# Kernel tuning notes

Hardware: AMD Instinct MI355X
Metric: run time of the kernel (lower is better)

## Reference

```python
import jax, jax.numpy as jnp
import numpy as np

DIM = 1024
CTX_DIM = 768
HEADS = 16
D_HEAD = 64
INNER = HEADS * D_HEAD  # 1024
EPS = 1e-5


def _layernorm(x, g, b):
    mu = jnp.mean(x, axis=-1, keepdims=True)
    var = jnp.mean(jnp.square(x - mu), axis=-1, keepdims=True)
    return (x - mu) * jax.lax.rsqrt(var + EPS) * g + b


def setup_inputs() -> dict:
    key = jax.random.key(0)
    ks = jax.random.split(key, 8)
    s = lambda fan_in: 1.0 / np.sqrt(fan_in)
    return {
        "x": jax.random.normal(ks[0], (4, 2048, DIM), dtype=jnp.float32),
        "context": jax.random.normal(ks[1], (4, 2048, CTX_DIM), dtype=jnp.float32),
        "norm_g": jnp.ones((DIM,), jnp.float32),
        "norm_b": jnp.zeros((DIM,), jnp.float32),
        "normc_g": jnp.ones((CTX_DIM,), jnp.float32),
        "normc_b": jnp.zeros((CTX_DIM,), jnp.float32),
        # Linear weights stored [in, out] so y = x @ W (bias=False as in module)
        "Wq": jax.random.uniform(ks[2], (DIM, INNER), jnp.float32, -s(DIM), s(DIM)),
        "Wk": jax.random.uniform(ks[3], (CTX_DIM, INNER), jnp.float32, -s(CTX_DIM), s(CTX_DIM)),
        "Wv": jax.random.uniform(ks[4], (CTX_DIM, INNER), jnp.float32, -s(CTX_DIM), s(CTX_DIM)),
        "Wo": jax.random.uniform(ks[5], (INNER, DIM), jnp.float32, -s(INNER), s(INNER)),
    }


def reference(x, context, norm_g, norm_b, normc_g, normc_b, Wq, Wk, Wv, Wo):
    b, n, _ = x.shape
    m = context.shape[1]
    xn = _layernorm(x, norm_g, norm_b)
    cn = _layernorm(context, normc_g, normc_b)
    # project and split heads: b n (h d) -> b h n d
    split = lambda t, L: t.reshape(b, L, HEADS, D_HEAD).transpose(0, 2, 1, 3)
    q = split(xn @ Wq, n)
    k = split(cn @ Wk, m)
    v = split(cn @ Wv, m)
    sim = jnp.einsum('bhid,bhjd->bhij', q, k) / np.sqrt(D_HEAD)
    attn = jax.nn.softmax(sim, axis=-1)  # dropout p=0 (eval): identity
    out = jnp.einsum('bhij,bhjd->bhid', attn, v)
    out = out.transpose(0, 2, 1, 3).reshape(b, n, INNER)
    return out @ Wo
```

## Files before the change

### kernel.cpp

```cpp
#include <hip/hip_runtime.h>
#include <hip/hip_bf16.h>
#include <stdint.h>

#define TOK 8192
#define NQ 2048
#define DIMX 1024
#define CTXD 768

typedef __attribute__((ext_vector_type(8))) short short8;
typedef __attribute__((ext_vector_type(4))) float f32x4;
typedef __attribute__((ext_vector_type(2))) unsigned int u32x2;

typedef __attribute__((address_space(3))) uint32_t lds_u32_t;
typedef const __attribute__((address_space(1))) uint32_t glb_u32_t;

__device__ __forceinline__ void gld_lds16(const void* g, void* l) {
  __builtin_amdgcn_global_load_lds((glb_u32_t*)g, (lds_u32_t*)l, 16, 0, 0);
}

__device__ __forceinline__ uint16_t f2bf(float f) {
  union { float f; uint32_t u; } v; v.f = f;
  uint32_t r = v.u + 0x7fffu + ((v.u >> 16) & 1u);
  return (uint16_t)(r >> 16);
}

__device__ __forceinline__ uint32_t cvt_pk_bf16(float lo, float hi) {
  uint32_t d;
  asm("v_cvt_pk_bf16_f32 %0, %1, %2" : "=v"(d) : "v"(lo), "v"(hi));
  return d;
}

__device__ __forceinline__ float fexp2(float x) {
#if __has_builtin(__builtin_amdgcn_exp2f)
  return __builtin_amdgcn_exp2f(x);
#else
  float d;
  asm volatile("v_exp_f32 %0, %1\n\ts_nop 1" : "=v"(d) : "v"(x));
  return d;
#endif
}

template<int COLS, int NW>
__global__ __launch_bounds__(COLS/4)
void ln_cast_kernel(const float* __restrict__ x, const float* __restrict__ g,
                    const float* __restrict__ b, uint16_t* __restrict__ out) {
  int row = blockIdx.x;
  int tid = threadIdx.x;
  const float* xr = x + (size_t)row * COLS + tid * 4;
  float4 v = *(const float4*)xr;
  float s1 = v.x + v.y + v.z + v.w;
  float s2 = v.x*v.x + v.y*v.y + v.z*v.z + v.w*v.w;
#pragma unroll
  for (int off = 1; off < 64; off <<= 1) {
    s1 += __shfl_xor(s1, off);
    s2 += __shfl_xor(s2, off);
  }
  __shared__ float sm[2][NW];
  int w = tid >> 6;
  if ((tid & 63) == 0) { sm[0][w] = s1; sm[1][w] = s2; }
  __syncthreads();
  float t1 = 0.f, t2 = 0.f;
#pragma unroll
  for (int i = 0; i < NW; i++) { t1 += sm[0][i]; t2 += sm[1][i]; }
  float mu = t1 * (1.0f / COLS);
  float var = t2 * (1.0f / COLS) - mu * mu;
  float rs = rsqrtf(var + 1e-5f);
  float4 gv = *(const float4*)(g + tid * 4);
  float4 bv = *(const float4*)(b + tid * 4);
  uint32_t lo = (uint32_t)f2bf((v.x - mu) * rs * gv.x + bv.x) |
                ((uint32_t)f2bf((v.y - mu) * rs * gv.y + bv.y) << 16);
  uint32_t hi = (uint32_t)f2bf((v.z - mu) * rs * gv.z + bv.z) |
                ((uint32_t)f2bf((v.w - mu) * rs * gv.w + bv.w) << 16);
  uint2 o; o.x = lo; o.y = hi;
  *(uint2*)(out + (size_t)row * COLS + tid * 4) = o;
}

__global__ __launch_bounds__(256)
void transpose_cast4_kernel(const float* __restrict__ W0, const float* __restrict__ W1,
                            const float* __restrict__ W2, const float* __restrict__ W3,
                            uint16_t* __restrict__ T0, uint16_t* __restrict__ T1,
                            uint16_t* __restrict__ T2, uint16_t* __restrict__ T3) {
  int z = blockIdx.z;
  const float* W = (z == 0) ? W0 : (z == 1) ? W1 : (z == 2) ? W2 : W3;
  uint16_t* WT   = (z == 0) ? T0 : (z == 1) ? T1 : (z == 2) ? T2 : T3;
  int K = (z == 1 || z == 2) ? CTXD : DIMX;
  const int N = DIMX;
  int c0 = blockIdx.x * 32, r0 = blockIdx.y * 32;
  if (r0 >= K) return;
  __shared__ float t[32][33];
  int tx = threadIdx.x & 31, ty = threadIdx.x >> 5;
#pragma unroll
  for (int i = 0; i < 4; i++)
    t[ty + 8*i][tx] = W[(size_t)(r0 + ty + 8*i) * N + c0 + tx];
  __syncthreads();
#pragma unroll
  for (int i = 0; i < 4; i++)
    WT[(size_t)(c0 + ty + 8*i) * K + r0 + tx] = f2bf(t[tx][ty + 8*i]);
}

__device__ __forceinline__ void gemm_block(
    const uint16_t* __restrict__ A, const uint16_t* __restrict__ BT,
    void* __restrict__ C, int N, int K, float oscale,
    int out_bf16, int permc, int m0, int n0,
    uint16_t* Al, uint16_t* Bl, int tid) {
  int l = tid & 63, w = tid >> 6;
  int g = l >> 4, r = l & 15;
  int wm = w >> 1, wn = w & 1;
  f32x4 acc[4][4] = {};
  int srow = tid >> 3, sslot = tid & 7;

  for (int kt = 0; kt < K; kt += 64) {
    __syncthreads();
#pragma unroll
    for (int c = 0; c < 4; c++) {
      int row = c * 32 + srow;
      int ksrc = (sslot * 8) ^ ((row & 7) << 3);
      gld_lds16(A + (size_t)(m0 + row) * K + kt + ksrc, Al + (c * 256 + w * 64) * 8);
    }
#pragma unroll
    for (int c = 0; c < 4; c++) {
      int row = c * 32 + srow;
      int ksrc = (sslot * 8) ^ ((row & 7) << 3);
      gld_lds16(BT + (size_t)(n0 + row) * K + kt + ksrc, Bl + (c * 256 + w * 64) * 8);
    }
    __syncthreads();
#pragma unroll
    for (int kk = 0; kk < 2; kk++) {
      int kb2 = (kk * 32 + g * 8) * 2;
      short8 af[4], bfr[4];
#pragma unroll
      for (int mf = 0; mf < 4; mf++) {
        int row = wm * 64 + mf * 16 + r;
        af[mf] = *(const short8*)((const char*)Al + row * 128 + (kb2 ^ ((row & 7) << 4)));
      }
#pragma unroll
      for (int nf = 0; nf < 4; nf++) {
        int row = wn * 64 + nf * 16 + r;
        bfr[nf] = *(const short8*)((const char*)Bl + row * 128 + (kb2 ^ ((row & 7) << 4)));
      }
#pragma unroll
      for (int mf = 0; mf < 4; mf++)
#pragma unroll
        for (int nf = 0; nf < 4; nf++)
          acc[mf][nf] = __builtin_amdgcn_mfma_f32_16x16x32_bf16(af[mf], bfr[nf], acc[mf][nf], 0, 0, 0);
    }
  }
#pragma unroll
  for (int mf = 0; mf < 4; mf++) {
#pragma unroll
    for (int i = 0; i < 4; i++) {
      size_t row = (size_t)m0 + wm * 64 + mf * 16 + g * 4 + i;
      if (permc) {
        u32x2 pk;
        pk.x = cvt_pk_bf16(acc[mf][0][i], acc[mf][1][i]);
        pk.y = cvt_pk_bf16(acc[mf][2][i], acc[mf][3][i]);
        *(u32x2*)((uint16_t*)C + row * N + n0 + wn * 64 + r * 4) = pk;
      } else {
#pragma unroll
        for (int nf = 0; nf < 4; nf++) {
          int col = n0 + wn * 64 + nf * 16 + r;
          float val = acc[mf][nf][i] * oscale;
          if (out_bf16) ((uint16_t*)C)[row * N + col] = f2bf(val);
          else          ((float*)C)[row * N + col] = val;
        }
      }
    }
  }
}

__global__ __launch_bounds__(256)
void gemm_proj3_kernel(const uint16_t* __restrict__ xn, const uint16_t* __restrict__ cn,
                       const uint16_t* __restrict__ WqT, const uint16_t* __restrict__ WkT,
                       const uint16_t* __restrict__ WvT,
                       uint16_t* __restrict__ Qs, uint16_t* __restrict__ Ks,
                       uint16_t* __restrict__ VTs, float qscale) {
  __shared__ __align__(16) uint16_t Al[128 * 64];
  __shared__ __align__(16) uint16_t Bl[128 * 64];
  int flat = blockIdx.x;
  flat = (flat & 7) * 192 + (flat >> 3);
  const uint16_t* A; const uint16_t* BT; uint16_t* C;
  int N, K, permc, m0, n0;
  float osc = 1.f;
  if (flat < 512) {
    A = xn; BT = WqT; C = Qs; N = DIMX; K = DIMX; permc = 0; osc = qscale;
    n0 = (flat & 7) * 128; m0 = (flat >> 3) * 128;
  } else if (flat < 1024) {
    int f = flat - 512;
    A = cn; BT = WkT; C = Ks; N = DIMX; K = CTXD; permc = 0;
    n0 = (f & 7) * 128; m0 = (f >> 3) * 128;
  } else {
    int f = flat - 1024;
    A = WvT; BT = cn; C = VTs; N = TOK; K = CTXD; permc = 1;
    n0 = (f & 63) * 128; m0 = (f >> 6) * 128;
  }
  gemm_block(A, BT, C, N, K, osc, 1, permc, m0, n0, Al, Bl, threadIdx.x);
}

__global__ __launch_bounds__(256)
void gemm_out_kernel(const uint16_t* __restrict__ A, const uint16_t* __restrict__ BT,
                     float* __restrict__ C, int M, int N, int K) {
  __shared__ __align__(16) uint16_t Al[128 * 64];
  __shared__ __align__(16) uint16_t Bl[128 * 64];
  int flat = blockIdx.y * gridDim.x + blockIdx.x;
  int nwg = gridDim.x * gridDim.y;
  flat = (flat & 7) * (nwg >> 3) + (flat >> 3);
  int bx = flat & (gridDim.x - 1);
  int by = flat / gridDim.x;
  gemm_block(A, BT, C, N, K, 1.f, 0, 0, by * 128, bx * 128, Al, Bl, threadIdx.x);
}

__global__ __launch_bounds__(256)
void attn_kernel(const uint16_t* __restrict__ Q, const uint16_t* __restrict__ Kp,
                 const uint16_t* __restrict__ VT, uint16_t* __restrict__ O) {
  __shared__ __align__(16) uint16_t Kl[64 * 64];
  __shared__ __align__(16) uint16_t Vl[64 * 64];
  __shared__ __align__(16) uint16_t Pl[4 * 32 * 64];
  int tid = threadIdx.x;
  int l = tid & 63, w = tid >> 6;
  int g = l >> 4, r = l & 15;
  int flat = blockIdx.y * 16 + blockIdx.x;
  flat = (flat & 7) * 128 + (flat >> 3);
  int q0 = (flat & 15) * 128;
  int bh = flat >> 4, b = bh >> 4, h = bh & 15;

  short8 qa[2][2];
#pragma unroll
  for (int qb = 0; qb < 2; qb++) {
    const uint16_t* qptr = Q + (size_t)(b * NQ + q0 + w * 32 + qb * 16 + r) * DIMX + h * 64;
    qa[qb][0] = *(const short8*)(qptr + g * 8);
    qa[qb][1] = *(const short8*)(qptr + 32 + g * 8);
  }

  float lpart[2][4] = {};
  f32x4 oacc[2][4] = {};

  const uint16_t* kbase = Kp + (size_t)(b * NQ) * DIMX + h * 64;
  const uint16_t* vbase = VT + (size_t)(h * 64) * TOK + b * NQ;
  int srow = tid >> 3, sslot = tid & 7;

  char* pwb = (char*)Pl + w * 4096;
  const char* prb = (const char*)Pl + w * 4096;

  for (int kv0 = 0; kv0 < NQ; kv0 += 64) {
    __syncthreads();
#pragma unroll
    for (int c = 0; c < 2; c++) {
      int key = c * 32 + srow;
      int dsrc = (sslot * 8) ^ ((key & 7) << 3);
      gld_lds16(kbase + (size_t)(kv0 + key) * DIMX + dsrc, Kl + (c * 256 + w * 64) * 8);
    }
#pragma unroll
    for (int c = 0; c < 2; c++) {
      int d = c * 32 + srow;
      int ksrc = (sslot * 8) ^ ((d & 7) << 3);
      gld_lds16(vbase + (size_t)d * TOK + kv0 + ksrc, Vl + (c * 256 + w * 64) * 8);
    }
    __syncthreads();

    f32x4 sc[2][4] = {};
    __builtin_amdgcn_s_setprio(1);
#pragma unroll
    for (int kk = 0; kk < 2; kk++) {
      int kb2 = (kk * 32 + g * 8) * 2;
#pragma unroll
      for (int c = 0; c < 4; c++) {
        int row = c * 16 + r;
        short8 kf = *(const short8*)((const char*)Kl + row * 128 + (kb2 ^ ((row & 7) << 4)));
        sc[0][c] = __builtin_amdgcn_mfma_f32_16x16x32_bf16(qa[0][kk], kf, sc[0][c], 0, 0, 0);
        sc[1][c] = __builtin_amdgcn_mfma_f32_16x16x32_bf16(qa[1][kk], kf, sc[1][c], 0, 0, 0);
      }
    }
    __builtin_amdgcn_s_setprio(0);

#pragma unroll
    for (int qb = 0; qb < 2; qb++) {
#pragma unroll
      for (int i = 0; i < 4; i++) {
        float p0 = fexp2(sc[qb][0][i]);
        float p1 = fexp2(sc[qb][1][i]);
        float p2 = fexp2(sc[qb][2][i]);
        float p3 = fexp2(sc[qb][3][i]);
        lpart[qb][i] += (p0 + p1) + (p2 + p3);
        u32x2 pk;
        pk.x = cvt_pk_bf16(p0, p1);
        pk.y = cvt_pk_bf16(p2, p3);
        int q = qb * 16 + g * 4 + i;
        *(u32x2*)(pwb + q * 128 + ((r * 8) ^ ((q & 7) << 4))) = pk;
      }
    }

    __builtin_amdgcn_s_setprio(1);
#pragma unroll
    for (int kk = 0; kk < 2; kk++) {
      int kb2 = (kk * 64 + g * 16);
      short8 pa0 = *(const short8*)(prb + (0 * 16 + r) * 128 + (kb2 ^ ((r & 7) << 4)));
      short8 pa1 = *(const short8*)(prb + (1 * 16 + r) * 128 + (kb2 ^ ((r & 7) << 4)));
#pragma unroll
      for (int c = 0; c < 4; c++) {
        int row = c * 16 + r;
        short8 vf = *(const short8*)((const char*)Vl + row * 128 + ((kk * 32 + g * 8) * 2 ^ ((row & 7) << 4)));
        oacc[0][c] = __builtin_amdgcn_mfma_f32_16x16x32_bf16(pa0, vf, oacc[0][c], 0, 0, 0);
        oacc[1][c] = __builtin_amdgcn_mfma_f32_16x16x32_bf16(pa1, vf, oacc[1][c], 0, 0, 0);
      }
    }
    __builtin_amdgcn_s_setprio(0);
  }

#pragma unroll
  for (int qb = 0; qb < 2; qb++)
#pragma unroll
    for (int i = 0; i < 4; i++) {
      lpart[qb][i] += __shfl_xor(lpart[qb][i], 1);
      lpart[qb][i] += __shfl_xor(lpart[qb][i], 2);
      lpart[qb][i] += __shfl_xor(lpart[qb][i], 4);
      lpart[qb][i] += __shfl_xor(lpart[qb][i], 8);
    }

#pragma unroll
  for (int qb = 0; qb < 2; qb++) {
    uint16_t* obase = O + (size_t)(b * NQ + q0 + w * 32 + qb * 16) * DIMX + h * 64;
#pragma unroll
    for (int i = 0; i < 4; i++) {
      float inv = 1.f / lpart[qb][i];
#pragma unroll
      for (int c = 0; c < 4; c++)
        obase[(size_t)(g * 4 + i) * DIMX + c * 16 + r] = f2bf(oacc[qb][c][i] * inv);
    }
  }
}

extern "C" void kernel_launch(void* const* d_in, const int* in_sizes, int n_in,
                              void* d_out, int out_size, void* d_ws, size_t ws_size,
                              hipStream_t stream) {
  (void)in_sizes; (void)n_in; (void)out_size; (void)ws_size;
  const float* x       = (const float*)d_in[0];
  const float* ctx     = (const float*)d_in[1];
  const float* norm_g  = (const float*)d_in[2];
  const float* norm_b  = (const float*)d_in[3];
  const float* normc_g = (const float*)d_in[4];
  const float* normc_b = (const float*)d_in[5];
  const float* Wq      = (const float*)d_in[6];
  const float* Wk      = (const float*)d_in[7];
  const float* Wv      = (const float*)d_in[8];
  const float* Wo      = (const float*)d_in[9];

  char* p = (char*)d_ws;
  uint16_t* xn  = (uint16_t*)p; p += (size_t)TOK * DIMX * 2;
  uint16_t* cn  = (uint16_t*)p; p += (size_t)TOK * CTXD * 2;
  uint16_t* WqT = (uint16_t*)p; p += (size_t)DIMX * DIMX * 2;
  uint16_t* WkT = (uint16_t*)p; p += (size_t)DIMX * CTXD * 2;
  uint16_t* WvT = (uint16_t*)p; p += (size_t)DIMX * CTXD * 2;
  uint16_t* WoT = (uint16_t*)p; p += (size_t)DIMX * DIMX * 2;
  uint16_t* Qs  = (uint16_t*)p; p += (size_t)TOK * DIMX * 2;
  uint16_t* Ks  = (uint16_t*)p; p += (size_t)TOK * DIMX * 2;
  uint16_t* VTs = (uint16_t*)p; p += (size_t)DIMX * TOK * 2;
  uint16_t* AO  = (uint16_t*)p; p += (size_t)TOK * DIMX * 2;

  ln_cast_kernel<DIMX, 4><<<TOK, 256, 0, stream>>>(x, norm_g, norm_b, xn);
  ln_cast_kernel<CTXD, 3><<<TOK, 192, 0, stream>>>(ctx, normc_g, normc_b, cn);

  transpose_cast4_kernel<<<dim3(DIMX/32, DIMX/32, 4), 256, 0, stream>>>(
      Wq, Wk, Wv, Wo, WqT, WkT, WvT, WoT);

  const float qscale = 0.125f * 1.44269504088896340736f;
  gemm_proj3_kernel<<<1536, 256, 0, stream>>>(xn, cn, WqT, WkT, WvT, Qs, Ks, VTs, qscale);

  attn_kernel<<<dim3(NQ/128, 64), 256, 0, stream>>>(Qs, Ks, VTs, AO);

  gemm_out_kernel<<<dim3(DIMX/128, TOK/128), 256, 0, stream>>>(AO, WoT, (float*)d_out, TOK, DIMX, DIMX);
}
```

Before: 206.4 us.

## Merge layernorm launches and use 128x64 tiles in output projection GEMM

The two layernorm launches become a single kernel over both x and context rows. For context rows, threads past the 768 columns sit idle. The output projection GEMM gets its own inline 128x64 tile loop instead of the shared 128x128 gemm_block, which doubles the workgroup count from 512 to 1024 so more CUs stay busy. The cost is more A-tile reloads from memory, and each workgroup does less compute per byte loaded.

```diff
diff --git a/kernel.cpp b/kernel.cpp
--- a/kernel.cpp
+++ b/kernel.cpp
@@ -40,14 +40,20 @@
 #endif
 }
 
-template<int COLS, int NW>
-__global__ __launch_bounds__(COLS/4)
-void ln_cast_kernel(const float* __restrict__ x, const float* __restrict__ g,
-                    const float* __restrict__ b, uint16_t* __restrict__ out) {
+__global__ __launch_bounds__(256)
+void ln_both_kernel(const float* __restrict__ x, const float* __restrict__ gx,
+                    const float* __restrict__ bx,
+                    const float* __restrict__ c, const float* __restrict__ gc,
+                    const float* __restrict__ bc,
+                    uint16_t* __restrict__ xn, uint16_t* __restrict__ cn) {
   int row = blockIdx.x;
   int tid = threadIdx.x;
-  const float* xr = x + (size_t)row * COLS + tid * 4;
-  float4 v = *(const float4*)xr;
+  const float *src, *g, *bb; uint16_t* dst; int COLS;
+  if (row < TOK) { src = x; g = gx; bb = bx; dst = xn; COLS = DIMX; }
+  else { row -= TOK; src = c; g = gc; bb = bc; dst = cn; COLS = CTXD; }
+  bool act = tid * 4 < COLS;
+  float4 v = make_float4(0.f, 0.f, 0.f, 0.f);
+  if (act) v = *(const float4*)(src + (size_t)row * COLS + tid * 4);
   float s1 = v.x + v.y + v.z + v.w;
   float s2 = v.x*v.x + v.y*v.y + v.z*v.z + v.w*v.w;
 #pragma unroll
@@ -55,24 +61,25 @@
     s1 += __shfl_xor(s1, off);
     s2 += __shfl_xor(s2, off);
   }
-  __shared__ float sm[2][NW];
+  __shared__ float sm[2][4];
   int w = tid >> 6;
   if ((tid & 63) == 0) { sm[0][w] = s1; sm[1][w] = s2; }
   __syncthreads();
-  float t1 = 0.f, t2 = 0.f;
-#pragma unroll
-  for (int i = 0; i < NW; i++) { t1 += sm[0][i]; t2 += sm[1][i]; }
-  float mu = t1 * (1.0f / COLS);
-  float var = t2 * (1.0f / COLS) - mu * mu;
+  float t1 = sm[0][0] + sm[0][1] + sm[0][2] + sm[0][3];
+  float t2 = sm[1][0] + sm[1][1] + sm[1][2] + sm[1][3];
+  float mu = t1 / COLS;
+  float var = t2 / COLS - mu * mu;
   float rs = rsqrtf(var + 1e-5f);
-  float4 gv = *(const float4*)(g + tid * 4);
-  float4 bv = *(const float4*)(b + tid * 4);
-  uint32_t lo = (uint32_t)f2bf((v.x - mu) * rs * gv.x + bv.x) |
-                ((uint32_t)f2bf((v.y - mu) * rs * gv.y + bv.y) << 16);
-  uint32_t hi = (uint32_t)f2bf((v.z - mu) * rs * gv.z + bv.z) |
-                ((uint32_t)f2bf((v.w - mu) * rs * gv.w + bv.w) << 16);
-  uint2 o; o.x = lo; o.y = hi;
-  *(uint2*)(out + (size_t)row * COLS + tid * 4) = o;
+  if (act) {
+    float4 gv = *(const float4*)(g + tid * 4);
+    float4 bv = *(const float4*)(bb + tid * 4);
+    uint32_t lo = (uint32_t)f2bf((v.x - mu) * rs * gv.x + bv.x) |
+                  ((uint32_t)f2bf((v.y - mu) * rs * gv.y + bv.y) << 16);
+    uint32_t hi = (uint32_t)f2bf((v.z - mu) * rs * gv.z + bv.z) |
+                  ((uint32_t)f2bf((v.w - mu) * rs * gv.w + bv.w) << 16);
+    uint2 o; o.x = lo; o.y = hi;
+    *(uint2*)(dst + (size_t)row * COLS + tid * 4) = o;
+  }
 }
 
 __global__ __launch_bounds__(256)
@@ -200,13 +207,68 @@
 void gemm_out_kernel(const uint16_t* __restrict__ A, const uint16_t* __restrict__ BT,
                      float* __restrict__ C, int M, int N, int K) {
   __shared__ __align__(16) uint16_t Al[128 * 64];
-  __shared__ __align__(16) uint16_t Bl[128 * 64];
+  __shared__ __align__(16) uint16_t Bl[64 * 64];
+  int tid = threadIdx.x;
+  int l = tid & 63, w = tid >> 6;
+  int g = l >> 4, r = l & 15;
+  int wm = w >> 1, wn = w & 1;
   int flat = blockIdx.y * gridDim.x + blockIdx.x;
   int nwg = gridDim.x * gridDim.y;
   flat = (flat & 7) * (nwg >> 3) + (flat >> 3);
-  int bx = flat & (gridDim.x - 1);
-  int by = flat / gridDim.x;
-  gemm_block(A, BT, C, N, K, 1.f, 0, 0, by * 128, bx * 128, Al, Bl, threadIdx.x);
+  int bx = flat & 15;
+  int by = flat >> 4;
+  int n0 = bx * 64, m0 = by * 128;
+  f32x4 acc[4][2] = {};
+  int srow = tid >> 3, sslot = tid & 7;
+
+  for (int kt = 0; kt < K; kt += 64) {
+    __syncthreads();
+#pragma unroll
+    for (int c = 0; c < 4; c++) {
+      int row = c * 32 + srow;
+      int ksrc = (sslot * 8) ^ ((row & 7) << 3);
+      gld_lds16(A + (size_t)(m0 + row) * K + kt + ksrc, Al + (c * 256 + w * 64) * 8);
+    }
+#pragma unroll
+    for (int c = 0; c < 2; c++) {
+      int row = c * 32 + srow;
+      int ksrc = (sslot * 8) ^ ((row & 7) << 3);
+      gld_lds16(BT + (size_t)(n0 + row) * K + kt + ksrc, Bl + (c * 256 + w * 64) * 8);
+    }
+    __syncthreads();
+#pragma unroll
+    for (int kk = 0; kk < 2; kk++) {
+      int kb2 = (kk * 32 + g * 8) * 2;
+      short8 af[4], bfr[2];
+#pragma unroll
+      for (int mf = 0; mf < 4; mf++) {
+        int row = wm * 64 + mf * 16 + r;
+        af[mf] = *(const short8*)((const char*)Al + row * 128 + (kb2 ^ ((row & 7) << 4)));
+      }
+#pragma unroll
+      for (int nf = 0; nf < 2; nf++) {
+        int row = wn * 32 + nf * 16 + r;
+        bfr[nf] = *(const short8*)((const char*)Bl + row * 128 + (kb2 ^ ((row & 7) << 4)));
+      }
+#pragma unroll
+      for (int mf = 0; mf < 4; mf++)
+#pragma unroll
+        for (int nf = 0; nf < 2; nf++)
+          acc[mf][nf] = __builtin_amdgcn_mfma_f32_16x16x32_bf16(af[mf], bfr[nf], acc[mf][nf], 0, 0, 0);
+    }
+  }
+#pragma unroll
+  for (int mf = 0; mf < 4; mf++) {
+#pragma unroll
+    for (int i = 0; i < 4; i++) {
+      size_t row = (size_t)m0 + wm * 64 + mf * 16 + g * 4 + i;
+#pragma unroll
+      for (int nf = 0; nf < 2; nf++) {
+        int col = n0 + wn * 32 + nf * 16 + r;
+        C[row * N + col] = acc[mf][nf][i];
+      }
+    }
+  }
 }
 
 __global__ __launch_bounds__(256)
@@ -356,8 +418,7 @@
   uint16_t* VTs = (uint16_t*)p; p += (size_t)DIMX * TOK * 2;
   uint16_t* AO  = (uint16_t*)p; p += (size_t)TOK * DIMX * 2;
 
-  ln_cast_kernel<DIMX, 4><<<TOK, 256, 0, stream>>>(x, norm_g, norm_b, xn);
-  ln_cast_kernel<CTXD, 3><<<TOK, 192, 0, stream>>>(ctx, normc_g, normc_b, cn);
+  ln_both_kernel<<<TOK * 2, 256, 0, stream>>>(x, norm_g, norm_b, ctx, normc_g, normc_b, xn, cn);
 
   transpose_cast4_kernel<<<dim3(DIMX/32, DIMX/32, 4), 256, 0, stream>>>(
       Wq, Wk, Wv, Wo, WqT, WkT, WvT, WoT);
@@ -367,5 +428,5 @@
 
   attn_kernel<<<dim3(NQ/128, 64), 256, 0, stream>>>(Qs, Ks, VTs, AO);
 
-  gemm_out_kernel<<<dim3(DIMX/128, TOK/128), 256, 0, stream>>>(AO, WoT, (float*)d_out, TOK, DIMX, DIMX);
-}
+  gemm_out_kernel<<<dim3(16, 64), 256, 0, stream>>>(AO, WoT, (float*)d_out, TOK, DIMX, DIMX);
+}
```

After: 208.3 us. No clear change (+1.0%).

## Keep attention probabilities in registers via transposed QK MFMA and merge layernorm launches

Applied to the files above, without the earlier changes.

The attention kernel now computes S^T by swapping the MFMA operands, so each lane holds the exponentiated scores in the layout the PV MFMA expects as its A operand. This removes the per-wave LDS staging buffer for P, its write/read traffic and the associated swizzle math. Row sums are reduced with a different shuffle pattern. The projection GEMM epilogue is changed to scattered 16-bit stores with a matching column permutation, and the two layernorm launches are merged into one kernel with masked lanes for the context rows. The scattered epilogue stores and idle threads in the context layernorm blocks are the trade-offs.

```diff
diff --git a/kernel.cpp b/kernel.cpp
--- a/kernel.cpp
+++ b/kernel.cpp
@@ -40,14 +40,20 @@
 #endif
 }
 
-template<int COLS, int NW>
-__global__ __launch_bounds__(COLS/4)
-void ln_cast_kernel(const float* __restrict__ x, const float* __restrict__ g,
-                    const float* __restrict__ b, uint16_t* __restrict__ out) {
+__global__ __launch_bounds__(256)
+void ln_both_kernel(const float* __restrict__ x, const float* __restrict__ gx,
+                    const float* __restrict__ bx,
+                    const float* __restrict__ c, const float* __restrict__ gc,
+                    const float* __restrict__ bc,
+                    uint16_t* __restrict__ xn, uint16_t* __restrict__ cn) {
   int row = blockIdx.x;
   int tid = threadIdx.x;
-  const float* xr = x + (size_t)row * COLS + tid * 4;
-  float4 v = *(const float4*)xr;
+  const float *src, *g, *bb; uint16_t* dst; int COLS;
+  if (row < TOK) { src = x; g = gx; bb = bx; dst = xn; COLS = DIMX; }
+  else { row -= TOK; src = c; g = gc; bb = bc; dst = cn; COLS = CTXD; }
+  bool act = tid * 4 < COLS;
+  float4 v = make_float4(0.f, 0.f, 0.f, 0.f);
+  if (act) v = *(const float4*)(src + (size_t)row * COLS + tid * 4);
   float s1 = v.x + v.y + v.z + v.w;
   float s2 = v.x*v.x + v.y*v.y + v.z*v.z + v.w*v.w;
 #pragma unroll
@@ -55,24 +61,25 @@
     s1 += __shfl_xor(s1, off);
     s2 += __shfl_xor(s2, off);
   }
-  __shared__ float sm[2][NW];
+  __shared__ float sm[2][4];
   int w = tid >> 6;
   if ((tid & 63) == 0) { sm[0][w] = s1; sm[1][w] = s2; }
   __syncthreads();
-  float t1 = 0.f, t2 = 0.f;
-#pragma unroll
-  for (int i = 0; i < NW; i++) { t1 += sm[0][i]; t2 += sm[1][i]; }
-  float mu = t1 * (1.0f / COLS);
-  float var = t2 * (1.0f / COLS) - mu * mu;
+  float t1 = sm[0][0] + sm[0][1] + sm[0][2] + sm[0][3];
+  float t2 = sm[1][0] + sm[1][1] + sm[1][2] + sm[1][3];
+  float mu = t1 / COLS;
+  float var = t2 / COLS - mu * mu;
   float rs = rsqrtf(var + 1e-5f);
-  float4 gv = *(const float4*)(g + tid * 4);
-  float4 bv = *(const float4*)(b + tid * 4);
-  uint32_t lo = (uint32_t)f2bf((v.x - mu) * rs * gv.x + bv.x) |
-                ((uint32_t)f2bf((v.y - mu) * rs * gv.y + bv.y) << 16);
-  uint32_t hi = (uint32_t)f2bf((v.z - mu) * rs * gv.z + bv.z) |
-                ((uint32_t)f2bf((v.w - mu) * rs * gv.w + bv.w) << 16);
-  uint2 o; o.x = lo; o.y = hi;
-  *(uint2*)(out + (size_t)row * COLS + tid * 4) = o;
+  if (act) {
+    float4 gv = *(const float4*)(g + tid * 4);
+    float4 bv = *(const float4*)(bb + tid * 4);
+    uint32_t lo = (uint32_t)f2bf((v.x - mu) * rs * gv.x + bv.x) |
+                  ((uint32_t)f2bf((v.y - mu) * rs * gv.y + bv.y) << 16);
+    uint32_t hi = (uint32_t)f2bf((v.z - mu) * rs * gv.z + bv.z) |
+                  ((uint32_t)f2bf((v.w - mu) * rs * gv.w + bv.w) << 16);
+    uint2 o; o.x = lo; o.y = hi;
+    *(uint2*)(dst + (size_t)row * COLS + tid * 4) = o;
+  }
 }
 
 __global__ __launch_bounds__(256)
@@ -151,10 +158,12 @@
     for (int i = 0; i < 4; i++) {
       size_t row = (size_t)m0 + wm * 64 + mf * 16 + g * 4 + i;
       if (permc) {
-        u32x2 pk;
-        pk.x = cvt_pk_bf16(acc[mf][0][i], acc[mf][1][i]);
-        pk.y = cvt_pk_bf16(acc[mf][2][i], acc[mf][3][i]);
-        *(u32x2*)((uint16_t*)C + row * N + n0 + wn * 64 + r * 4) = pk;
+        int pbase = ((r >> 3) << 4) | (((r >> 2) & 1) << 3) | (r & 3);
+        uint16_t* cb = (uint16_t*)C + row * N + n0 + wn * 64;
+        cb[pbase +  0] = f2bf(acc[mf][0][i]);
+        cb[pbase +  4] = f2bf(acc[mf][1][i]);
+        cb[pbase + 32] = f2bf(acc[mf][2][i]);
+        cb[pbase + 36] = f2bf(acc[mf][3][i]);
       } else {
 #pragma unroll
         for (int nf = 0; nf < 4; nf++) {
@@ -214,7 +223,6 @@
                  const uint16_t* __restrict__ VT, uint16_t* __restrict__ O) {
   __shared__ __align__(16) uint16_t Kl[64 * 64];
   __shared__ __align__(16) uint16_t Vl[64 * 64];
-  __shared__ __align__(16) uint16_t Pl[4 * 32 * 64];
   int tid = threadIdx.x;
   int l = tid & 63, w = tid >> 6;
   int g = l >> 4, r = l & 15;
@@ -231,15 +239,12 @@
     qa[qb][1] = *(const short8*)(qptr + 32 + g * 8);
   }
 
-  float lpart[2][4] = {};
+  float lpart[2] = {0.f, 0.f};
   f32x4 oacc[2][4] = {};
 
   const uint16_t* kbase = Kp + (size_t)(b * NQ) * DIMX + h * 64;
   const uint16_t* vbase = VT + (size_t)(h * 64) * TOK + b * NQ;
   int srow = tid >> 3, sslot = tid & 7;
-
-  char* pwb = (char*)Pl + w * 4096;
-  const char* prb = (const char*)Pl + w * 4096;
 
   for (int kv0 = 0; kv0 < NQ; kv0 += 64) {
     __syncthreads();
@@ -266,62 +271,61 @@
       for (int c = 0; c < 4; c++) {
         int row = c * 16 + r;
         short8 kf = *(const short8*)((const char*)Kl + row * 128 + (kb2 ^ ((row & 7) << 4)));
-        sc[0][c] = __builtin_amdgcn_mfma_f32_16x16x32_bf16(qa[0][kk], kf, sc[0][c], 0, 0, 0);
-        sc[1][c] = __builtin_amdgcn_mfma_f32_16x16x32_bf16(qa[1][kk], kf, sc[1][c], 0, 0, 0);
+        sc[0][c] = __builtin_amdgcn_mfma_f32_16x16x32_bf16(kf, qa[0][kk], sc[0][c], 0, 0, 0);
+        sc[1][c] = __builtin_amdgcn_mfma_f32_16x16x32_bf16(kf, qa[1][kk], sc[1][c], 0, 0, 0);
       }
     }
     __builtin_amdgcn_s_setprio(0);
 
+    short8 pa[2][2];
 #pragma unroll
     for (int qb = 0; qb < 2; qb++) {
-#pragma unroll
-      for (int i = 0; i < 4; i++) {
-        float p0 = fexp2(sc[qb][0][i]);
-        float p1 = fexp2(sc[qb][1][i]);
-        float p2 = fexp2(sc[qb][2][i]);
-        float p3 = fexp2(sc[qb][3][i]);
-        lpart[qb][i] += (p0 + p1) + (p2 + p3);
-        u32x2 pk;
-        pk.x = cvt_pk_bf16(p0, p1);
-        pk.y = cvt_pk_bf16(p2, p3);
-        int q = qb * 16 + g * 4 + i;
-        *(u32x2*)(pwb + q * 128 + ((r * 8) ^ ((q & 7) << 4))) = pk;
+      float pe[4][4];
+#pragma unroll
+      for (int c = 0; c < 4; c++)
+#pragma unroll
+        for (int i = 0; i < 4; i++) {
+          pe[c][i] = fexp2(sc[qb][c][i]);
+          lpart[qb] += pe[c][i];
+        }
+#pragma unroll
+      for (int kk = 0; kk < 2; kk++) {
+        union { uint32_t u[4]; short8 s; } pk;
+        pk.u[0] = cvt_pk_bf16(pe[kk * 2][0], pe[kk * 2][1]);
+        pk.u[1] = cvt_pk_bf16(pe[kk * 2][2], pe[kk * 2][3]);
+        pk.u[2] = cvt_pk_bf16(pe[kk * 2 + 1][0], pe[kk * 2 + 1][1]);
+        pk.u[3] = cvt_pk_bf16(pe[kk * 2 + 1][2], pe[kk * 2 + 1][3]);
+        pa[qb][kk] = pk.s;
       }
     }
 
     __builtin_amdgcn_s_setprio(1);
 #pragma unroll
     for (int kk = 0; kk < 2; kk++) {
-      int kb2 = (kk * 64 + g * 16);
-      short8 pa0 = *(const short8*)(prb + (0 * 16 + r) * 128 + (kb2 ^ ((r & 7) << 4)));
-      short8 pa1 = *(const short8*)(prb + (1 * 16 + r) * 128 + (kb2 ^ ((r & 7) << 4)));
 #pragma unroll
       for (int c = 0; c < 4; c++) {
         int row = c * 16 + r;
-        short8 vf = *(const short8*)((const char*)Vl + row * 128 + ((kk * 32 + g * 8) * 2 ^ ((row & 7) << 4)));
-        oacc[0][c] = __builtin_amdgcn_mfma_f32_16x16x32_bf16(pa0, vf, oacc[0][c], 0, 0, 0);
-        oacc[1][c] = __builtin_amdgcn_mfma_f32_16x16x32_bf16(pa1, vf, oacc[1][c], 0, 0, 0);
+        short8 vf = *(const short8*)((const char*)Vl + row * 128 + (((kk * 32 + g * 8) * 2) ^ ((row & 7) << 4)));
+        oacc[0][c] = __builtin_amdgcn_mfma_f32_16x16x32_bf16(pa[0][kk], vf, oacc[0][c], 0, 0, 0);
+        oacc[1][c] = __builtin_amdgcn_mfma_f32_16x16x32_bf16(pa[1][kk], vf, oacc[1][c], 0, 0, 0);
       }
     }
     __builtin_amdgcn_s_setprio(0);
   }
 
 #pragma unroll
-  for (int qb = 0; qb < 2; qb++)
-#pragma unroll
-    for (int i = 0; i < 4; i++) {
-      lpart[qb][i] += __shfl_xor(lpart[qb][i], 1);
-      lpart[qb][i] += __shfl_xor(lpart[qb][i], 2);
-      lpart[qb][i] += __shfl_xor(lpart[qb][i], 4);
-      lpart[qb][i] += __shfl_xor(lpart[qb][i], 8);
-    }
+  for (int qb = 0; qb < 2; qb++) {
+    lpart[qb] += __shfl_xor(lpart[qb], 16);
+    lpart[qb] += __shfl_xor(lpart[qb], 32);
+  }
 
 #pragma unroll
   for (int qb = 0; qb < 2; qb++) {
     uint16_t* obase = O + (size_t)(b * NQ + q0 + w * 32 + qb * 16) * DIMX + h * 64;
 #pragma unroll
     for (int i = 0; i < 4; i++) {
-      float inv = 1.f / lpart[qb][i];
+      float li = __shfl(lpart[qb], g * 4 + i);
+      float inv = 1.f / li;
 #pragma unroll
       for (int c = 0; c < 4; c++)
         obase[(size_t)(g * 4 + i) * DIMX + c * 16 + r] = f2bf(oacc[qb][c][i] * inv);
@@ -356,8 +360,7 @@
   uint16_t* VTs = (uint16_t*)p; p += (size_t)DIMX * TOK * 2;
   uint16_t* AO  = (uint16_t*)p; p += (size_t)TOK * DIMX * 2;
 
-  ln_cast_kernel<DIMX, 4><<<TOK, 256, 0, stream>>>(x, norm_g, norm_b, xn);
-  ln_cast_kernel<CTXD, 3><<<TOK, 192, 0, stream>>>(ctx, normc_g, normc_b, cn);
+  ln_both_kernel<<<TOK * 2, 256, 0, stream>>>(x, norm_g, norm_b, ctx, normc_g, normc_b, xn, cn);
 
   transpose_cast4_kernel<<<dim3(DIMX/32, DIMX/32, 4), 256, 0, stream>>>(
       Wq, Wk, Wv, Wo, WqT, WkT, WvT, WoT);
```

Result: faster. 199.6 us (-3.3%).
